# Performance work log

Hardware: AMD Instinct MI355X
Metric: run time of the kernel (lower is better)

## Reference

```python
import jax, jax.numpy as jnp
import numpy as np

# multi-scale pyramid (low2high: lowest resolution first), d_model etc. from module defaults
SHAPES = ((8, 8), (16, 16), (32, 32), (64, 64))
D, HEADS, DH, PTS, NLV, NLAYERS, DFF = 256, 8, 32, 4, 4, 6, 1024
L_TOTAL = sum(h * w for h, w in SHAPES)  # 5440
B = 4


def _ref_points():
    # normalized (x, y) pixel centers per level, concatenated -> [L_TOTAL, 2]
    pts = []
    for (H, W) in SHAPES:
        ry = (jnp.arange(H, dtype=jnp.float32) + 0.5) / H
        rx = (jnp.arange(W, dtype=jnp.float32) + 0.5) / W
        gy, gx = jnp.meshgrid(ry, rx, indexing='ij')
        pts.append(jnp.stack([gx.ravel(), gy.ravel()], -1))
    return jnp.concatenate(pts, 0)


def _lev_ids():
    return jnp.concatenate([jnp.full((h * w,), l, dtype=jnp.int32)
                            for l, (h, w) in enumerate(SHAPES)])


def _layer_norm(x, g, b):
    m = jnp.mean(x, -1, keepdims=True)
    v = jnp.mean((x - m) ** 2, -1, keepdims=True)
    return g * (x - m) * jax.lax.rsqrt(v + 1e-5) + b


def _ms_deform_attn(q, src, ref, w_off, b_off, w_attn, b_attn, w_val, b_val, w_out, b_out):
    Bq, L, _ = q.shape
    v = (src @ w_val + b_val).reshape(Bq, L, HEADS, DH)
    off = (q @ w_off + b_off).reshape(Bq, L, HEADS, NLV, PTS, 2)
    aw = jax.nn.softmax((q @ w_attn + b_attn).reshape(Bq, L, HEADS, NLV * PTS), -1)
    aw = aw.reshape(Bq, L, HEADS, NLV, PTS)
    # offset normalizer is (W, H) per level
    norm = jnp.array([[w, h] for (h, w) in SHAPES], dtype=q.dtype)
    loc = ref[None, :, None, None, None, :] + off / norm[None, None, None, :, None, :]
    out = jnp.zeros((Bq, L, HEADS, DH), q.dtype)
    start = 0
    for l, (H_, W_) in enumerate(SHAPES):
        vl = v[:, start:start + H_ * W_].transpose(0, 2, 1, 3)  # [B, heads, HW, dh]
        # grid_sample(align_corners=False): pixel coord = loc * size - 0.5
        x = loc[:, :, :, l, :, 0] * W_ - 0.5  # [B, L, heads, P]
        y = loc[:, :, :, l, :, 1] * H_ - 0.5
        x0 = jnp.floor(x).astype(jnp.int32)
        y0 = jnp.floor(y).astype(jnp.int32)
        fx = x - x0
        fy = y - y0

        def corner(ix, iy, w):
            inb = ((ix >= 0) & (ix < W_) & (iy >= 0) & (iy < H_)).astype(q.dtype)
            idx = jnp.clip(iy, 0, H_ - 1) * W_ + jnp.clip(ix, 0, W_ - 1)
            idx = idx.transpose(0, 2, 1, 3).reshape(Bq, HEADS, L * PTS, 1)
            g = jnp.take_along_axis(vl, idx, axis=2)  # [B, heads, L*P, dh]
            wt = (w * inb).transpose(0, 2, 1, 3).reshape(Bq, HEADS, L * PTS, 1)
            return g * wt

        samp = (corner(x0, y0, (1 - fx) * (1 - fy))
                + corner(x0 + 1, y0, fx * (1 - fy))
                + corner(x0, y0 + 1, (1 - fx) * fy)
                + corner(x0 + 1, y0 + 1, fx * fy))
        samp = samp.reshape(Bq, HEADS, L, PTS, DH)
        out = out + jnp.einsum('blhp,bhlpd->blhd', aw[:, :, :, l, :], samp)
        start += H_ * W_
    return out.reshape(Bq, L, D) @ w_out + b_out


def setup_inputs() -> dict:
    key = jax.random.key(0)
    ks = jax.random.split(key, 16)
    s = 0.02
    inp = {
        'src': jax.random.normal(ks[0], (B, L_TOTAL, D), jnp.float32),
        'pos': jax.random.normal(ks[1], (B, L_TOTAL, D), jnp.float32),
        'level_embed': jax.random.normal(ks[2], (NLV, D), jnp.float32),
        'w_off': jax.random.normal(ks[3], (NLAYERS, D, HEADS * NLV * PTS * 2), jnp.float32) * s,
        'b_off': jnp.zeros((NLAYERS, HEADS * NLV * PTS * 2), jnp.float32),
        'w_attn': jax.random.normal(ks[4], (NLAYERS, D, HEADS * NLV * PTS), jnp.float32) * s,
        'b_attn': jnp.zeros((NLAYERS, HEADS * NLV * PTS), jnp.float32),
        'w_val': jax.random.normal(ks[5], (NLAYERS, D, D), jnp.float32) * s,
        'b_val': jnp.zeros((NLAYERS, D), jnp.float32),
        'w_out': jax.random.normal(ks[6], (NLAYERS, D, D), jnp.float32) * s,
        'b_out': jnp.zeros((NLAYERS, D), jnp.float32),
        'ln1_g': jnp.ones((NLAYERS, D), jnp.float32),
        'ln1_b': jnp.zeros((NLAYERS, D), jnp.float32),
        'w_ff1': jax.random.normal(ks[7], (NLAYERS, D, DFF), jnp.float32) * s,
        'b_ff1': jnp.zeros((NLAYERS, DFF), jnp.float32),
        'w_ff2': jax.random.normal(ks[8], (NLAYERS, DFF, D), jnp.float32) * s,
        'b_ff2': jnp.zeros((NLAYERS, D), jnp.float32),
        'ln2_g': jnp.ones((NLAYERS, D), jnp.float32),
        'ln2_b': jnp.zeros((NLAYERS, D), jnp.float32),
    }
    return inp


def reference(src, pos, level_embed, w_off, b_off, w_attn, b_attn, w_val, b_val,
              w_out, b_out, ln1_g, ln1_b, w_ff1, b_ff1, w_ff2, b_ff2, ln2_g, ln2_b):
    # lvl_pos_embed = pos + level_embed[level-of-token] (masks all False -> valid_ratios == 1)
    lvl_pos = pos + level_embed[_lev_ids()]
    ref = _ref_points().astype(src.dtype)
    x = src
    for i in range(NLAYERS):
        q = x + lvl_pos
        x2 = _ms_deform_attn(q, x, ref, w_off[i], b_off[i], w_attn[i], b_attn[i],
                             w_val[i], b_val[i], w_out[i], b_out[i])
        x = _layer_norm(x + x2, ln1_g[i], ln1_b[i])
        ff = jax.nn.relu(x @ w_ff1[i] + b_ff1[i]) @ w_ff2[i] + b_ff2[i]
        x = _layer_norm(x + ff, ln2_g[i], ln2_b[i])
    return x
```

## Files before the change

kernel.cpp:

```cpp
#include <hip/hip_runtime.h>

#define LTOT 5440
#define NTOK 21760

typedef float  f32x4  __attribute__((ext_vector_type(4)));
typedef float  f32x2  __attribute__((ext_vector_type(2)));
typedef short  short8 __attribute__((ext_vector_type(8)));

__device__ __forceinline__ unsigned short f2bf(float f) {
  unsigned int u = __float_as_uint(f);
  u += 0x7FFF + ((u >> 16) & 1);
  return (unsigned short)(u >> 16);
}

__global__ void wconv(const float* __restrict__ w_off, const float* __restrict__ w_attn,
                      const float* __restrict__ w_val, const float* __restrict__ w_out,
                      const float* __restrict__ w_ff1, const float* __restrict__ w_ff2,
                      unsigned short* __restrict__ dst) {
  int tid = blockIdx.x * 256 + threadIdx.x;
  const int PER = 753664;
  if (tid >= 6 * PER) return;
  int layer = tid / PER;
  int rem = tid - layer * PER;
  int base, K, N;
  const float* src;
  if (rem < 65536)       { base = 0;      K = 256;  N = 256;  src = w_off; }
  else if (rem < 98304)  { base = 65536;  K = 256;  N = 128;  src = w_attn; }
  else if (rem < 163840) { base = 98304;  K = 256;  N = 256;  src = w_val; }
  else if (rem < 229376) { base = 163840; K = 256;  N = 256;  src = w_out; }
  else if (rem < 491520) { base = 229376; K = 256;  N = 1024; src = w_ff1; }
  else                   { base = 491520; K = 1024; N = 256;  src = w_ff2; }
  int local = rem - base;
  int n = local / K, k = local - n * K;
  dst[tid] = f2bf(src[(size_t)layer * K * N + (size_t)k * N + n]);
}

__global__ void bpack(const float* __restrict__ b_off, const float* __restrict__ b_attn,
                      float* __restrict__ fb) {
  int l = blockIdx.x, t = threadIdx.x;
  fb[l * 384 + t] = (t < 256) ? b_off[l * 256 + t] : b_attn[l * 128 + t - 256];
}

__global__ void prep(const float* __restrict__ src, const float* __restrict__ pos,
                     const float* __restrict__ lev_emb, float* __restrict__ x,
                     unsigned short* __restrict__ xb, unsigned short* __restrict__ qb) {
  int i = blockIdx.x * 256 + threadIdx.x;
  int d4 = i & 63;
  int tok = (i >> 6) % LTOT;
  int lev = (tok < 64) ? 0 : (tok < 320) ? 1 : (tok < 1344) ? 2 : 3;
  float4 s = ((const float4*)src)[i];
  float4 pv = ((const float4*)pos)[i];
  float4 lv = ((const float4*)lev_emb)[lev * 64 + d4];
  ((float4*)x)[i] = s;
  ushort4 o;
  o.x = f2bf(s.x); o.y = f2bf(s.y); o.z = f2bf(s.z); o.w = f2bf(s.w);
  ((ushort4*)xb)[i] = o;
  ushort4 q;
  q.x = f2bf(s.x + pv.x + lv.x);
  q.y = f2bf(s.y + pv.y + lv.y);
  q.z = f2bf(s.z + pv.z + lv.z);
  q.w = f2bf(s.w + pv.w + lv.w);
  ((ushort4*)qb)[i] = q;
}

template<bool RELU, bool OBF16>
__global__ __launch_bounds__(256) void gemm_tn(
    const unsigned short* __restrict__ A, const unsigned short* __restrict__ Wt,
    const float* __restrict__ bias, void* __restrict__ Cout,
    int M, int N, int K) {
  __shared__ __align__(16) unsigned short a_lds[128 * 64];
  __shared__ __align__(16) unsigned short b_lds[128 * 64];
  int m0 = blockIdx.x * 128;
  int n0 = blockIdx.y * 128;
  int t = threadIdx.x;
  int w = t >> 6, l = t & 63;
  int wr = (w >> 1) * 64, wc = (w & 1) * 64;
  int lr = l & 15, lk = (l >> 4) * 8;

  f32x4 acc[4][4] = {};

  for (int k0 = 0; k0 < K; k0 += 64) {
#pragma unroll
    for (int i = 0; i < 4; ++i) {
      int c = i * 256 + t;
      int row = c >> 3, off8 = (c & 7) * 8;
      const unsigned short* gp = A + (size_t)(m0 + row) * K + k0 + off8;
      __builtin_amdgcn_global_load_lds(
          (const __attribute__((address_space(1))) void*)gp,
          (__attribute__((address_space(3))) void*)(a_lds + c * 8), 16, 0, 0);
    }
#pragma unroll
    for (int i = 0; i < 4; ++i) {
      int c = i * 256 + t;
      int row = c >> 3, off8 = (c & 7) * 8;
      const unsigned short* gp = Wt + (size_t)(n0 + row) * K + k0 + off8;
      __builtin_amdgcn_global_load_lds(
          (const __attribute__((address_space(1))) void*)gp,
          (__attribute__((address_space(3))) void*)(b_lds + c * 8), 16, 0, 0);
    }
    __syncthreads();
#pragma unroll
    for (int kk = 0; kk < 64; kk += 32) {
      short8 af[4], bfr[4];
#pragma unroll
      for (int m = 0; m < 4; ++m)
        af[m] = *(const short8*)(a_lds + (wr + m * 16 + lr) * 64 + kk + lk);
#pragma unroll
      for (int n = 0; n < 4; ++n)
        bfr[n] = *(const short8*)(b_lds + (wc + n * 16 + lr) * 64 + kk + lk);
#pragma unroll
      for (int m = 0; m < 4; ++m)
#pragma unroll
        for (int n = 0; n < 4; ++n)
          acc[m][n] = __builtin_amdgcn_mfma_f32_16x16x32_bf16(af[m], bfr[n], acc[m][n], 0, 0, 0);
    }
    __syncthreads();
  }

  int rb = (l >> 4) * 4;
#pragma unroll
  for (int n = 0; n < 4; ++n) {
    int col = n0 + wc + n * 16 + lr;
    float bv = bias[col];
#pragma unroll
    for (int m = 0; m < 4; ++m) {
#pragma unroll
      for (int r = 0; r < 4; ++r) {
        int row = m0 + wr + m * 16 + rb + r;
        float v = acc[m][n][r] + bv;
        if (RELU) v = fmaxf(v, 0.0f);
        if (OBF16) ((unsigned short*)Cout)[(size_t)row * N + col] = f2bf(v);
        else       ((float*)Cout)[(size_t)row * N + col] = v;
      }
    }
  }
}

template<bool RELU, bool OBF16>
__global__ __launch_bounds__(256) void gemm_tn64(
    const unsigned short* __restrict__ A, const unsigned short* __restrict__ Wt,
    const float* __restrict__ bias, void* __restrict__ Cout,
    int M, int N, int K) {
  __shared__ __align__(16) unsigned short a_lds[64 * 64];
  __shared__ __align__(16) unsigned short b_lds[128 * 64];
  int m0 = blockIdx.x * 64;
  int n0 = blockIdx.y * 128;
  int t = threadIdx.x;
  int w = t >> 6, l = t & 63;
  int wr = (w >> 1) * 32, wc = (w & 1) * 64;
  int lr = l & 15, lk = (l >> 4) * 8;

  f32x4 acc[2][4] = {};

  for (int k0 = 0; k0 < K; k0 += 64) {
#pragma unroll
    for (int i = 0; i < 2; ++i) {
      int c = i * 256 + t;
      int row = c >> 3, off8 = (c & 7) * 8;
      const unsigned short* gp = A + (size_t)(m0 + row) * K + k0 + off8;
      __builtin_amdgcn_global_load_lds(
          (const __attribute__((address_space(1))) void*)gp,
          (__attribute__((address_space(3))) void*)(a_lds + c * 8), 16, 0, 0);
    }
#pragma unroll
    for (int i = 0; i < 4; ++i) {
      int c = i * 256 + t;
      int row = c >> 3, off8 = (c & 7) * 8;
      const unsigned short* gp = Wt + (size_t)(n0 + row) * K + k0 + off8;
      __builtin_amdgcn_global_load_lds(
          (const __attribute__((address_space(1))) void*)gp,
          (__attribute__((address_space(3))) void*)(b_lds + c * 8), 16, 0, 0);
    }
    __syncthreads();
#pragma unroll
    for (int kk = 0; kk < 64; kk += 32) {
      short8 af[2], bfr[4];
#pragma unroll
      for (int m = 0; m < 2; ++m)
        af[m] = *(const short8*)(a_lds + (wr + m * 16 + lr) * 64 + kk + lk);
#pragma unroll
      for (int n = 0; n < 4; ++n)
        bfr[n] = *(const short8*)(b_lds + (wc + n * 16 + lr) * 64 + kk + lk);
#pragma unroll
      for (int m = 0; m < 2; ++m)
#pragma unroll
        for (int n = 0; n < 4; ++n)
          acc[m][n] = __builtin_amdgcn_mfma_f32_16x16x32_bf16(af[m], bfr[n], acc[m][n], 0, 0, 0);
    }
    __syncthreads();
  }

  int rb = (l >> 4) * 4;
#pragma unroll
  for (int n = 0; n < 4; ++n) {
    int col = n0 + wc + n * 16 + lr;
    float bv = bias[col];
#pragma unroll
    for (int m = 0; m < 2; ++m) {
#pragma unroll
      for (int r = 0; r < 4; ++r) {
        int row = m0 + wr + m * 16 + rb + r;
        float v = acc[m][n][r] + bv;
        if (RELU) v = fmaxf(v, 0.0f);
        if (OBF16) ((unsigned short*)Cout)[(size_t)row * N + col] = f2bf(v);
        else       ((float*)Cout)[(size_t)row * N + col] = v;
      }
    }
  }
}

__global__ __launch_bounds__(256) void gemm_proj(
    const unsigned short* __restrict__ qb, const unsigned short* __restrict__ xb,
    const unsigned short* __restrict__ wOA, const unsigned short* __restrict__ wV,
    const float* __restrict__ bOA, const float* __restrict__ bV,
    float* __restrict__ offat, unsigned short* __restrict__ vb) {
  __shared__ __align__(16) unsigned short a_lds[128 * 64];
  __shared__ __align__(16) unsigned short b_lds[128 * 64];
  const int K = 256;
  int by = blockIdx.y;
  bool isV = (by >= 3);
  const unsigned short* A  = isV ? xb : qb;
  const unsigned short* Wt = isV ? wV : wOA;
  const float* bias        = isV ? bV : bOA;
  int N  = isV ? 256 : 384;
  int n0 = (isV ? (by - 3) : by) * 128;
  int m0 = blockIdx.x * 128;
  int t = threadIdx.x;
  int w = t >> 6, l = t & 63;
  int wr = (w >> 1) * 64, wc = (w & 1) * 64;
  int lr = l & 15, lk = (l >> 4) * 8;

  f32x4 acc[4][4] = {};

  for (int k0 = 0; k0 < K; k0 += 64) {
#pragma unroll
    for (int i = 0; i < 4; ++i) {
      int c = i * 256 + t;
      int row = c >> 3, off8 = (c & 7) * 8;
      const unsigned short* gp = A + (size_t)(m0 + row) * K + k0 + off8;
      __builtin_amdgcn_global_load_lds(
          (const __attribute__((address_space(1))) void*)gp,
          (__attribute__((address_space(3))) void*)(a_lds + c * 8), 16, 0, 0);
    }
#pragma unroll
    for (int i = 0; i < 4; ++i) {
      int c = i * 256 + t;
      int row = c >> 3, off8 = (c & 7) * 8;
      const unsigned short* gp = Wt + (size_t)(n0 + row) * K + k0 + off8;
      __builtin_amdgcn_global_load_lds(
          (const __attribute__((address_space(1))) void*)gp,
          (__attribute__((address_space(3))) void*)(b_lds + c * 8), 16, 0, 0);
    }
    __syncthreads();
#pragma unroll
    for (int kk = 0; kk < 64; kk += 32) {
      short8 af[4], bfr[4];
#pragma unroll
      for (int m = 0; m < 4; ++m)
        af[m] = *(const short8*)(a_lds + (wr + m * 16 + lr) * 64 + kk + lk);
#pragma unroll
      for (int n = 0; n < 4; ++n)
        bfr[n] = *(const short8*)(b_lds + (wc + n * 16 + lr) * 64 + kk + lk);
#pragma unroll
      for (int m = 0; m < 4; ++m)
#pragma unroll
        for (int n = 0; n < 4; ++n)
          acc[m][n] = __builtin_amdgcn_mfma_f32_16x16x32_bf16(af[m], bfr[n], acc[m][n], 0, 0, 0);
    }
    __syncthreads();
  }

  int rb = (l >> 4) * 4;
#pragma unroll
  for (int n = 0; n < 4; ++n) {
    int col = n0 + wc + n * 16 + lr;
    float bv = bias[col];
#pragma unroll
    for (int m = 0; m < 4; ++m) {
#pragma unroll
      for (int r = 0; r < 4; ++r) {
        int row = m0 + wr + m * 16 + rb + r;
        float v = acc[m][n][r] + bv;
        if (isV) vb[(size_t)row * 256 + col] = f2bf(v);
        else     offat[(size_t)row * 384 + col] = v;
      }
    }
  }
}

__global__ __launch_bounds__(256) void ms_sample(
    const float* __restrict__ offattn, const unsigned short* __restrict__ vb,
    unsigned short* __restrict__ samp) {
  __shared__ __align__(16) uint2 sWI[512];
  int bid = blockIdx.x;
  int bl = (bid & 7) * (NTOK / 8) + (bid >> 3);
  int t = threadIdx.x;
  int l = bl % LTOT;
  int bbase = (bl - l) * 256;
  if (t < 128) {
    float logit = offattn[(size_t)bl * 384 + 256 + t];
    float mx = logit;
#pragma unroll
    for (int o = 1; o < 16; o <<= 1) mx = fmaxf(mx, __shfl_xor(mx, o));
    float e = __expf(logit - mx);
    float ssum = e;
#pragma unroll
    for (int o = 1; o < 16; o <<= 1) ssum += __shfl_xor(ssum, o);
    float aw = e / ssum;

    int lev = (t >> 2) & 3;
    int lev_q = (l < 64) ? 0 : (l < 320) ? 1 : (l < 1344) ? 2 : 3;
    int start_q = (lev_q == 0) ? 0 : (lev_q == 1) ? 64 : (lev_q == 2) ? 320 : 1344;
    int shq = lev_q + 3;
    int r = l - start_q;
    int Wq = 1 << shq;
    int iy = r >> shq, ix = r & (Wq - 1);
    float invWq = 1.0f / (float)Wq;
    float refx = ((float)ix + 0.5f) * invWq;
    float refy = ((float)iy + 0.5f) * invWq;
    int iW = 8 << lev;
    float Wl = (float)iW;
    int start_l = (lev == 0) ? 0 : (lev == 1) ? 64 : (lev == 2) ? 320 : 1344;
    float ox = offattn[(size_t)bl * 384 + 2 * t];
    float oy = offattn[(size_t)bl * 384 + 2 * t + 1];
    float gx = refx * Wl + ox - 0.5f;
    float gy = refy * Wl + oy - 0.5f;
    float flx = floorf(gx), fly = floorf(gy);
    int x0 = (int)flx, y0 = (int)fly;
    float fx = gx - flx, fy = gy - fly;
#pragma unroll
    for (int c = 0; c < 4; ++c) {
      int cx = x0 + (c & 1);
      int cy = y0 + (c >> 1);
      int inb = (cx >= 0) && (cx < iW) && (cy >= 0) && (cy < iW);
      int cxc = cx < 0 ? 0 : (cx > iW - 1 ? iW - 1 : cx);
      int cyc = cy < 0 ? 0 : (cy > iW - 1 ? iW - 1 : cy);
      float wx = (c & 1) ? fx : 1.0f - fx;
      float wy = (c & 2) ? fy : 1.0f - fy;
      float wgt = inb ? aw * wx * wy : 0.0f;
      unsigned int idxb = (unsigned int)(start_l + cyc * iW + cxc) * 512u;
      sWI[t * 4 + c] = make_uint2(__float_as_uint(wgt), idxb);
    }
  }
  __syncthreads();
  int h = t >> 5, j = t & 31;
  int q = j >> 3, p = j & 7;
  int rotp = ((h & 1) << 2) | q;
  const uint2* wiBase = sWI + h * 64 + q * 16;
  unsigned int chb = (unsigned int)(h * 32 + p * 4) * 2u;
  const char* vB = (const char*)(vb + bbase);
  uint4 wi[8];
#pragma unroll
  for (int kp = 0; kp < 8; ++kp) {
    int kq = ((kp + rotp) & 7) * 2;
    wi[kp] = *(const uint4*)(wiBase + kq);
  }
  uint2 u0[8], u1[8];
#pragma unroll
  for (int kp = 0; kp < 8; ++kp) {
    u0[kp] = *(const uint2*)(vB + (wi[kp].y + chb));
    u1[kp] = *(const uint2*)(vB + (wi[kp].w + chb));
  }
  f32x2 a01 = {0.0f, 0.0f}, a23 = {0.0f, 0.0f};
#pragma unroll
  for (int kp = 0; kp < 8; ++kp) {
    float w0 = __uint_as_float(wi[kp].x);
    float w1 = __uint_as_float(wi[kp].z);
    f32x2 w0v = {w0, w0}, w1v = {w1, w1};
    f32x2 va = { __uint_as_float(u0[kp].x << 16), __uint_as_float(u0[kp].x & 0xffff0000u) };
    f32x2 vbv = { __uint_as_float(u0[kp].y << 16), __uint_as_float(u0[kp].y & 0xffff0000u) };
    a01 = __builtin_elementwise_fma(w0v, va, a01);
    a23 = __builtin_elementwise_fma(w0v, vbv, a23);
    f32x2 vc = { __uint_as_float(u1[kp].x << 16), __uint_as_float(u1[kp].x & 0xffff0000u) };
    f32x2 vd = { __uint_as_float(u1[kp].y << 16), __uint_as_float(u1[kp].y & 0xffff0000u) };
    a01 = __builtin_elementwise_fma(w1v, vc, a01);
    a23 = __builtin_elementwise_fma(w1v, vd, a23);
  }
  float c0 = a01.x, c1 = a01.y, c2 = a23.x, c3 = a23.y;
  c0 += __shfl_xor(c0, 8);  c1 += __shfl_xor(c1, 8);
  c2 += __shfl_xor(c2, 8);  c3 += __shfl_xor(c3, 8);
  c0 += __shfl_xor(c0, 16); c1 += __shfl_xor(c1, 16);
  c2 += __shfl_xor(c2, 16); c3 += __shfl_xor(c3, 16);
  if (q == 0) {
    uint2 pk;
    pk.x = (unsigned int)f2bf(c0) | ((unsigned int)f2bf(c1) << 16);
    pk.y = (unsigned int)f2bf(c2) | ((unsigned int)f2bf(c3) << 16);
    *(uint2*)(samp + (size_t)bl * 256 + h * 32 + p * 4) = pk;
  }
}

template<bool QADD>
__global__ __launch_bounds__(256) void ln_fused(
    const float* __restrict__ xin, const float* __restrict__ yin,
    const float* __restrict__ g, const float* __restrict__ bb,
    const float* __restrict__ pos, const float* __restrict__ lev_emb,
    float* __restrict__ xout, unsigned short* __restrict__ xbout,
    unsigned short* __restrict__ qbout) {
  int row = blockIdx.x * 4 + (threadIdx.x >> 6);
  int lane = threadIdx.x & 63;
  size_t base = (size_t)row * 64 + lane;
  float4 xv = ((const float4*)xin)[base];
  float4 yv = ((const float4*)yin)[base];
  float4 tv;
  tv.x = xv.x + yv.x; tv.y = xv.y + yv.y; tv.z = xv.z + yv.z; tv.w = xv.w + yv.w;
  float s = tv.x + tv.y + tv.z + tv.w;
  float s2 = tv.x * tv.x + tv.y * tv.y + tv.z * tv.z + tv.w * tv.w;
#pragma unroll
  for (int o = 1; o < 64; o <<= 1) {
    s += __shfl_xor(s, o, 64);
    s2 += __shfl_xor(s2, o, 64);
  }
  float mean = s * (1.0f / 256.0f);
  float var = s2 * (1.0f / 256.0f) - mean * mean;
  float rstd = rsqrtf(var + 1e-5f);
  float4 gv = ((const float4*)g)[lane];
  float4 bv = ((const float4*)bb)[lane];
  float4 o;
  o.x = gv.x * (tv.x - mean) * rstd + bv.x;
  o.y = gv.y * (tv.y - mean) * rstd + bv.y;
  o.z = gv.z * (tv.z - mean) * rstd + bv.z;
  o.w = gv.w * (tv.w - mean) * rstd + bv.w;
  ((float4*)xout)[base] = o;
  ushort4 ob;
  ob.x = f2bf(o.x); ob.y = f2bf(o.y); ob.z = f2bf(o.z); ob.w = f2bf(o.w);
  ((ushort4*)xbout)[base] = ob;
  if (QADD) {
    int tok = row % LTOT;
    int lev = (tok < 64) ? 0 : (tok < 320) ? 1 : (tok < 1344) ? 2 : 3;
    float4 pv = ((const float4*)pos)[base];
    float4 lv = ((const float4*)lev_emb)[lev * 64 + lane];
    ushort4 q;
    q.x = f2bf(o.x + pv.x + lv.x);
    q.y = f2bf(o.y + pv.y + lv.y);
    q.z = f2bf(o.z + pv.z + lv.z);
    q.w = f2bf(o.w + pv.w + lv.w);
    ((ushort4*)qbout)[base] = q;
  }
}

extern "C" void kernel_launch(void* const* d_in, const int* in_sizes, int n_in,
                              void* d_out, int out_size, void* d_ws, size_t ws_size,
                              hipStream_t stream) {
  (void)in_sizes; (void)n_in; (void)out_size; (void)ws_size;
  const float* src     = (const float*)d_in[0];
  const float* pos     = (const float*)d_in[1];
  const float* lev_emb = (const float*)d_in[2];
  const float* w_off   = (const float*)d_in[3];
  const float* b_off   = (const float*)d_in[4];
  const float* w_attn  = (const float*)d_in[5];
  const float* b_attn  = (const float*)d_in[6];
  const float* w_val   = (const float*)d_in[7];
  const float* b_val   = (const float*)d_in[8];
  const float* w_out   = (const float*)d_in[9];
  const float* b_out   = (const float*)d_in[10];
  const float* ln1_g   = (const float*)d_in[11];
  const float* ln1_b   = (const float*)d_in[12];
  const float* w_ff1   = (const float*)d_in[13];
  const float* b_ff1   = (const float*)d_in[14];
  const float* w_ff2   = (const float*)d_in[15];
  const float* b_ff2   = (const float*)d_in[16];
  const float* ln2_g   = (const float*)d_in[17];
  const float* ln2_b   = (const float*)d_in[18];

  char* ws = (char*)d_ws;
  float*          x     = (float*)(ws + 0);
  float*          y     = (float*)(ws + 22282240);
  unsigned short* xb    = (unsigned short*)(ws + 44564480);
  unsigned short* qb    = (unsigned short*)(ws + 55705600);
  unsigned short* sampb = (unsigned short*)(ws + 55705600);
  float*          offat = (float*)(ws + 66846720);
  unsigned short* vb    = (unsigned short*)(ws + 100270080);
  unsigned short* h1    = (unsigned short*)(ws + 66846720);
  unsigned short* wT    = (unsigned short*)(ws + 111411200);
  float*          fb    = (float*)(ws + 120455168);

  wconv<<<17664, 256, 0, stream>>>(w_off, w_attn, w_val, w_out, w_ff1, w_ff2, wT);
  bpack<<<6, 384, 0, stream>>>(b_off, b_attn, fb);
  prep<<<5440, 256, 0, stream>>>(src, pos, lev_emb, x, xb, qb);

  for (int i = 0; i < 6; ++i) {
    const unsigned short* wl = wT + (size_t)i * 753664;
    gemm_proj<<<dim3(170, 5), 256, 0, stream>>>(qb, xb, wl + 0, wl + 98304,
                                                fb + i * 384, b_val + i * 256,
                                                offat, vb);
    ms_sample<<<NTOK, 256, 0, stream>>>(offat, vb, sampb);
    gemm_tn64<false, false><<<dim3(340, 2), 256, 0, stream>>>(sampb, wl + 163840, b_out + i * 256, (void*)y, NTOK, 256, 256);
    ln_fused<false><<<5440, 256, 0, stream>>>(x, y, ln1_g + i * 256, ln1_b + i * 256, pos, lev_emb, x, xb, qb);
    gemm_tn<true, true ><<<dim3(170, 8), 256, 0, stream>>>(xb, wl + 229376, b_ff1 + i * 1024, (void*)h1, NTOK, 1024, 256);
    gemm_tn64<false, false><<<dim3(340, 2), 256, 0, stream>>>(h1, wl + 491520, b_ff2 + i * 256, (void*)y, NTOK, 256, 1024);
    float* xo = (i == 5) ? (float*)d_out : x;
    if (i < 5)
      ln_fused<true ><<<5440, 256, 0, stream>>>(x, y, ln2_g + i * 256, ln2_b + i * 256, pos, lev_emb, xo, xb, qb);
    else
      ln_fused<false><<<5440, 256, 0, stream>>>(x, y, ln2_g + i * 256, ln2_b + i * 256, pos, lev_emb, xo, xb, qb);
  }
}
```

Before: 1.201 ms.

## Double-buffer GEMM LDS tiles with BK=32 prefetch and tune sampler scheduling

Each of the three bf16 MFMA GEMM kernels now splits K into 32-wide stages held in two LDS buffers. The next stage is fetched with global_load_lds while the current one runs through MFMA, with one barrier per stage instead of two per 64-wide step. The aim is to hide global-load latency behind compute, at the cost of twice as many barriers per unit of K and a shorter MFMA run between them. The sampling kernel also gets an occupancy hint in its launch bounds and sched_barriers that keep its gather loads grouped together.

```diff
diff --git a/kernel.cpp b/kernel.cpp
--- a/kernel.cpp
+++ b/kernel.cpp
@@ -12,6 +12,10 @@
   u += 0x7FFF + ((u >> 16) & 1);
   return (unsigned short)(u >> 16);
 }
+
+#define GLL16(gp, lp) __builtin_amdgcn_global_load_lds( \
+    (const __attribute__((address_space(1))) void*)(gp), \
+    (__attribute__((address_space(3))) void*)(lp), 16, 0, 0)
 
 __global__ void wconv(const float* __restrict__ w_off, const float* __restrict__ w_attn,
                       const float* __restrict__ w_val, const float* __restrict__ w_out,
@@ -68,8 +72,8 @@
     const unsigned short* __restrict__ A, const unsigned short* __restrict__ Wt,
     const float* __restrict__ bias, void* __restrict__ Cout,
     int M, int N, int K) {
-  __shared__ __align__(16) unsigned short a_lds[128 * 64];
-  __shared__ __align__(16) unsigned short b_lds[128 * 64];
+  __shared__ __align__(16) unsigned short a_lds[2][128 * 32];
+  __shared__ __align__(16) unsigned short b_lds[2][128 * 32];
   int m0 = blockIdx.x * 128;
   int n0 = blockIdx.y * 128;
   int t = threadIdx.x;
@@ -78,43 +82,54 @@
   int lr = l & 15, lk = (l >> 4) * 8;
 
   f32x4 acc[4][4] = {};
-
-  for (int k0 = 0; k0 < K; k0 += 64) {
-#pragma unroll
-    for (int i = 0; i < 4; ++i) {
-      int c = i * 256 + t;
-      int row = c >> 3, off8 = (c & 7) * 8;
-      const unsigned short* gp = A + (size_t)(m0 + row) * K + k0 + off8;
-      __builtin_amdgcn_global_load_lds(
-          (const __attribute__((address_space(1))) void*)gp,
-          (__attribute__((address_space(3))) void*)(a_lds + c * 8), 16, 0, 0);
-    }
-#pragma unroll
-    for (int i = 0; i < 4; ++i) {
-      int c = i * 256 + t;
-      int row = c >> 3, off8 = (c & 7) * 8;
-      const unsigned short* gp = Wt + (size_t)(n0 + row) * K + k0 + off8;
-      __builtin_amdgcn_global_load_lds(
-          (const __attribute__((address_space(1))) void*)gp,
-          (__attribute__((address_space(3))) void*)(b_lds + c * 8), 16, 0, 0);
-    }
+  int nt = K >> 5;
+  int cur = 0;
+
+#pragma unroll
+  for (int i = 0; i < 2; ++i) {
+    int c = i * 256 + t;
+    int row = c >> 2, s8 = (c & 3) * 8;
+    GLL16(A + (size_t)(m0 + row) * K + s8, a_lds[0] + c * 8);
+  }
+#pragma unroll
+  for (int i = 0; i < 2; ++i) {
+    int c = i * 256 + t;
+    int row = c >> 2, s8 = (c & 3) * 8;
+    GLL16(Wt + (size_t)(n0 + row) * K + s8, b_lds[0] + c * 8);
+  }
+  __syncthreads();
+
+  for (int tt = 0; tt < nt; ++tt) {
+    if (tt + 1 < nt) {
+      int k0 = (tt + 1) << 5;
+      int nxt = cur ^ 1;
+#pragma unroll
+      for (int i = 0; i < 2; ++i) {
+        int c = i * 256 + t;
+        int row = c >> 2, s8 = (c & 3) * 8;
+        GLL16(A + (size_t)(m0 + row) * K + k0 + s8, a_lds[nxt] + c * 8);
+      }
+#pragma unroll
+      for (int i = 0; i < 2; ++i) {
+        int c = i * 256 + t;
+        int row = c >> 2, s8 = (c & 3) * 8;
+        GLL16(Wt + (size_t)(n0 + row) * K + k0 + s8, b_lds[nxt] + c * 8);
+      }
+    }
+    short8 af[4], bfr[4];
+#pragma unroll
+    for (int m = 0; m < 4; ++m)
+      af[m] = *(const short8*)(a_lds[cur] + (wr + m * 16 + lr) * 32 + lk);
+#pragma unroll
+    for (int n = 0; n < 4; ++n)
+      bfr[n] = *(const short8*)(b_lds[cur] + (wc + n * 16 + lr) * 32 + lk);
+#pragma unroll
+    for (int m = 0; m < 4; ++m)
+#pragma unroll
+      for (int n = 0; n < 4; ++n)
+        acc[m][n] = __builtin_amdgcn_mfma_f32_16x16x32_bf16(af[m], bfr[n], acc[m][n], 0, 0, 0);
     __syncthreads();
-#pragma unroll
-    for (int kk = 0; kk < 64; kk += 32) {
-      short8 af[4], bfr[4];
-#pragma unroll
-      for (int m = 0; m < 4; ++m)
-        af[m] = *(const short8*)(a_lds + (wr + m * 16 + lr) * 64 + kk + lk);
-#pragma unroll
-      for (int n = 0; n < 4; ++n)
-        bfr[n] = *(const short8*)(b_lds + (wc + n * 16 + lr) * 64 + kk + lk);
-#pragma unroll
-      for (int m = 0; m < 4; ++m)
-#pragma unroll
-        for (int n = 0; n < 4; ++n)
-          acc[m][n] = __builtin_amdgcn_mfma_f32_16x16x32_bf16(af[m], bfr[n], acc[m][n], 0, 0, 0);
-    }
-    __syncthreads();
+    cur ^= 1;
   }
 
   int rb = (l >> 4) * 4;
@@ -141,8 +156,8 @@
     const unsigned short* __restrict__ A, const unsigned short* __restrict__ Wt,
     const float* __restrict__ bias, void* __restrict__ Cout,
     int M, int N, int K) {
-  __shared__ __align__(16) unsigned short a_lds[64 * 64];
-  __shared__ __align__(16) unsigned short b_lds[128 * 64];
+  __shared__ __align__(16) unsigned short a_lds[2][64 * 32];
+  __shared__ __align__(16) unsigned short b_lds[2][128 * 32];
   int m0 = blockIdx.x * 64;
   int n0 = blockIdx.y * 128;
   int t = threadIdx.x;
@@ -151,43 +166,48 @@
   int lr = l & 15, lk = (l >> 4) * 8;
 
   f32x4 acc[2][4] = {};
-
-  for (int k0 = 0; k0 < K; k0 += 64) {
+  int nt = K >> 5;
+  int cur = 0;
+
+  {
+    int row = t >> 2, s8 = (t & 3) * 8;
+    GLL16(A + (size_t)(m0 + row) * K + s8, a_lds[0] + t * 8);
 #pragma unroll
     for (int i = 0; i < 2; ++i) {
       int c = i * 256 + t;
-      int row = c >> 3, off8 = (c & 7) * 8;
-      const unsigned short* gp = A + (size_t)(m0 + row) * K + k0 + off8;
-      __builtin_amdgcn_global_load_lds(
-          (const __attribute__((address_space(1))) void*)gp,
-          (__attribute__((address_space(3))) void*)(a_lds + c * 8), 16, 0, 0);
-    }
-#pragma unroll
-    for (int i = 0; i < 4; ++i) {
-      int c = i * 256 + t;
-      int row = c >> 3, off8 = (c & 7) * 8;
-      const unsigned short* gp = Wt + (size_t)(n0 + row) * K + k0 + off8;
-      __builtin_amdgcn_global_load_lds(
-          (const __attribute__((address_space(1))) void*)gp,
-          (__attribute__((address_space(3))) void*)(b_lds + c * 8), 16, 0, 0);
-    }
+      int rw = c >> 2, sb = (c & 3) * 8;
+      GLL16(Wt + (size_t)(n0 + rw) * K + sb, b_lds[0] + c * 8);
+    }
+  }
+  __syncthreads();
+
+  for (int tt = 0; tt < nt; ++tt) {
+    if (tt + 1 < nt) {
+      int k0 = (tt + 1) << 5;
+      int nxt = cur ^ 1;
+      int row = t >> 2, s8 = (t & 3) * 8;
+      GLL16(A + (size_t)(m0 + row) * K + k0 + s8, a_lds[nxt] + t * 8);
+#pragma unroll
+      for (int i = 0; i < 2; ++i) {
+        int c = i * 256 + t;
+        int rw = c >> 2, sb = (c & 3) * 8;
+        GLL16(Wt + (size_t)(n0 + rw) * K + k0 + sb, b_lds[nxt] + c * 8);
+      }
+    }
+    short8 af[2], bfr[4];
+#pragma unroll
+    for (int m = 0; m < 2; ++m)
+      af[m] = *(const short8*)(a_lds[cur] + (wr + m * 16 + lr) * 32 + lk);
+#pragma unroll
+    for (int n = 0; n < 4; ++n)
+      bfr[n] = *(const short8*)(b_lds[cur] + (wc + n * 16 + lr) * 32 + lk);
+#pragma unroll
+    for (int m = 0; m < 2; ++m)
+#pragma unroll
+      for (int n = 0; n < 4; ++n)
+        acc[m][n] = __builtin_amdgcn_mfma_f32_16x16x32_bf16(af[m], bfr[n], acc[m][n], 0, 0, 0);
     __syncthreads();
-#pragma unroll
-    for (int kk = 0; kk < 64; kk += 32) {
-      short8 af[2], bfr[4];
-#pragma unroll
-      for (int m = 0; m < 2; ++m)
-        af[m] = *(const short8*)(a_lds + (wr + m * 16 + lr) * 64 + kk + lk);
-#pragma unroll
-      for (int n = 0; n < 4; ++n)
-        bfr[n] = *(const short8*)(b_lds + (wc + n * 16 + lr) * 64 + kk + lk);
-#pragma unroll
-      for (int m = 0; m < 2; ++m)
-#pragma unroll
-        for (int n = 0; n < 4; ++n)
-          acc[m][n] = __builtin_amdgcn_mfma_f32_16x16x32_bf16(af[m], bfr[n], acc[m][n], 0, 0, 0);
-    }
-    __syncthreads();
+    cur ^= 1;
   }
 
   int rb = (l >> 4) * 4;
@@ -214,15 +234,14 @@
     const unsigned short* __restrict__ wOA, const unsigned short* __restrict__ wV,
     const float* __restrict__ bOA, const float* __restrict__ bV,
     float* __restrict__ offat, unsigned short* __restrict__ vb) {
-  __shared__ __align__(16) unsigned short a_lds[128 * 64];
-  __shared__ __align__(16) unsigned short b_lds[128 * 64];
+  __shared__ __align__(16) unsigned short a_lds[2][128 * 32];
+  __shared__ __align__(16) unsigned short b_lds[2][128 * 32];
   const int K = 256;
   int by = blockIdx.y;
   bool isV = (by >= 3);
   const unsigned short* A  = isV ? xb : qb;
   const unsigned short* Wt = isV ? wV : wOA;
   const float* bias        = isV ? bV : bOA;
-  int N  = isV ? 256 : 384;
   int n0 = (isV ? (by - 3) : by) * 128;
   int m0 = blockIdx.x * 128;
   int t = threadIdx.x;
@@ -231,43 +250,54 @@
   int lr = l & 15, lk = (l >> 4) * 8;
 
   f32x4 acc[4][4] = {};
-
-  for (int k0 = 0; k0 < K; k0 += 64) {
-#pragma unroll
-    for (int i = 0; i < 4; ++i) {
-      int c = i * 256 + t;
-      int row = c >> 3, off8 = (c & 7) * 8;
-      const unsigned short* gp = A + (size_t)(m0 + row) * K + k0 + off8;
-      __builtin_amdgcn_global_load_lds(
-          (const __attribute__((address_space(1))) void*)gp,
-          (__attribute__((address_space(3))) void*)(a_lds + c * 8), 16, 0, 0);
-    }
-#pragma unroll
-    for (int i = 0; i < 4; ++i) {
-      int c = i * 256 + t;
-      int row = c >> 3, off8 = (c & 7) * 8;
-      const unsigned short* gp = Wt + (size_t)(n0 + row) * K + k0 + off8;
-      __builtin_amdgcn_global_load_lds(
-          (const __attribute__((address_space(1))) void*)gp,
-          (__attribute__((address_space(3))) void*)(b_lds + c * 8), 16, 0, 0);
-    }
+  const int nt = 8;
+  int cur = 0;
+
+#pragma unroll
+  for (int i = 0; i < 2; ++i) {
+    int c = i * 256 + t;
+    int row = c >> 2, s8 = (c & 3) * 8;
+    GLL16(A + (size_t)(m0 + row) * K + s8, a_lds[0] + c * 8);
+  }
+#pragma unroll
+  for (int i = 0; i < 2; ++i) {
+    int c = i * 256 + t;
+    int row = c >> 2, s8 = (c & 3) * 8;
+    GLL16(Wt + (size_t)(n0 + row) * K + s8, b_lds[0] + c * 8);
+  }
+  __syncthreads();
+
+  for (int tt = 0; tt < nt; ++tt) {
+    if (tt + 1 < nt) {
+      int k0 = (tt + 1) << 5;
+      int nxt = cur ^ 1;
+#pragma unroll
+      for (int i = 0; i < 2; ++i) {
+        int c = i * 256 + t;
+        int row = c >> 2, s8 = (c & 3) * 8;
+        GLL16(A + (size_t)(m0 + row) * K + k0 + s8, a_lds[nxt] + c * 8);
+      }
+#pragma unroll
+      for (int i = 0; i < 2; ++i) {
+        int c = i * 256 + t;
+        int row = c >> 2, s8 = (c & 3) * 8;
+        GLL16(Wt + (size_t)(n0 + row) * K + k0 + s8, b_lds[nxt] + c * 8);
+      }
+    }
+    short8 af[4], bfr[4];
+#pragma unroll
+    for (int m = 0; m < 4; ++m)
+      af[m] = *(const short8*)(a_lds[cur] + (wr + m * 16 + lr) * 32 + lk);
+#pragma unroll
+    for (int n = 0; n < 4; ++n)
+      bfr[n] = *(const short8*)(b_lds[cur] + (wc + n * 16 + lr) * 32 + lk);
+#pragma unroll
+    for (int m = 0; m < 4; ++m)
+#pragma unroll
+      for (int n = 0; n < 4; ++n)
+        acc[m][n] = __builtin_amdgcn_mfma_f32_16x16x32_bf16(af[m], bfr[n], acc[m][n], 0, 0, 0);
     __syncthreads();
-#pragma unroll
-    for (int kk = 0; kk < 64; kk += 32) {
-      short8 af[4], bfr[4];
-#pragma unroll
-      for (int m = 0; m < 4; ++m)
-        af[m] = *(const short8*)(a_lds + (wr + m * 16 + lr) * 64 + kk + lk);
-#pragma unroll
-      for (int n = 0; n < 4; ++n)
-        bfr[n] = *(const short8*)(b_lds + (wc + n * 16 + lr) * 64 + kk + lk);
-#pragma unroll
-      for (int m = 0; m < 4; ++m)
-#pragma unroll
-        for (int n = 0; n < 4; ++n)
-          acc[m][n] = __builtin_amdgcn_mfma_f32_16x16x32_bf16(af[m], bfr[n], acc[m][n], 0, 0, 0);
-    }
-    __syncthreads();
+    cur ^= 1;
   }
 
   int rb = (l >> 4) * 4;
@@ -288,7 +318,7 @@
   }
 }
 
-__global__ __launch_bounds__(256) void ms_sample(
+__global__ __launch_bounds__(256, 4) void ms_sample(
     const float* __restrict__ offattn, const unsigned short* __restrict__ vb,
     unsigned short* __restrict__ samp) {
   __shared__ __align__(16) uint2 sWI[512];
@@ -355,12 +385,14 @@
     int kq = ((kp + rotp) & 7) * 2;
     wi[kp] = *(const uint4*)(wiBase + kq);
   }
+  __builtin_amdgcn_sched_barrier(0);
   uint2 u0[8], u1[8];
 #pragma unroll
   for (int kp = 0; kp < 8; ++kp) {
     u0[kp] = *(const uint2*)(vB + (wi[kp].y + chb));
     u1[kp] = *(const uint2*)(vB + (wi[kp].w + chb));
   }
+  __builtin_amdgcn_sched_barrier(0);
   f32x2 a01 = {0.0f, 0.0f}, a23 = {0.0f, 0.0f};
 #pragma unroll
   for (int kp = 0; kp < 8; ++kp) {
```

Result: slower. 1.258 ms (+4.8%).
